# Kernel tuning notes

Measured on AMD Instinct MI355X. Metric: run time of the kernel, lower is better.

Reference implementation:

```python
import jax, jax.numpy as jnp
import numpy as np

HID, OUT = 128, 16
N_USER, N_MOVIE, N_DIR = 200000, 100000, 20000
ALPHA, NUM_LAYERS = 0.01, 2


def _seg_mean(h_src, src, dst, n_dst):
    # copy_u + mean reduce: mean of incoming messages per dst node (0 if no in-edges)
    msg = h_src[src]                                   # [E, H] gather
    s = jax.ops.segment_sum(msg, dst, num_segments=n_dst)
    deg = jax.ops.segment_sum(jnp.ones((dst.shape[0],), h_src.dtype), dst, num_segments=n_dst)
    return s / jnp.maximum(deg, 1.0)[:, None]


def setup_inputs() -> dict:
    key = jax.random.key(0)
    ks = jax.random.split(key, 16)
    inp = {
        'x_user': jax.random.normal(ks[0], (N_USER, 128), jnp.float32),
        'x_movie': jax.random.normal(ks[1], (N_MOVIE, 128), jnp.float32),
        'x_director': jax.random.normal(ks[2], (N_DIR, 128), jnp.float32),
        'rates_src': jax.random.randint(ks[3], (600000,), 0, N_USER, jnp.int32),
        'rates_dst': jax.random.randint(ks[4], (600000,), 0, N_MOVIE, jnp.int32),
        'rby_src': jax.random.randint(ks[5], (600000,), 0, N_MOVIE, jnp.int32),
        'rby_dst': jax.random.randint(ks[6], (600000,), 0, N_USER, jnp.int32),
        'dir_src': jax.random.randint(ks[7], (100000,), 0, N_DIR, jnp.int32),
        'dir_dst': jax.random.randint(ks[8], (100000,), 0, N_MOVIE, jnp.int32),
        'dby_src': jax.random.randint(ks[9], (100000,), 0, N_MOVIE, jnp.int32),
        'dby_dst': jax.random.randint(ks[10], (100000,), 0, N_DIR, jnp.int32),
    }
    sc = 1.0 / np.sqrt(128.0)
    inp['W_user'] = jax.random.normal(ks[11], (HID, 128), jnp.float32) * sc
    inp['b_user'] = jnp.zeros((HID,), jnp.float32)
    inp['W_movie'] = jax.random.normal(ks[12], (HID, 128), jnp.float32) * sc
    inp['b_movie'] = jnp.zeros((HID,), jnp.float32)
    inp['W_director'] = jax.random.normal(ks[13], (HID, 128), jnp.float32) * sc
    inp['b_director'] = jnp.zeros((HID,), jnp.float32)
    inp['W_out'] = jax.random.normal(ks[14], (OUT, HID), jnp.float32) * (1.0 / np.sqrt(HID))
    inp['b_out'] = jnp.zeros((OUT,), jnp.float32)
    return inp


def reference(x_user, x_movie, x_director,
              W_user, b_user, W_movie, b_movie, W_director, b_director,
              W_out, b_out,
              rates_src, rates_dst, rby_src, rby_dst,
              dir_src, dir_dst, dby_src, dby_dst):
    # per-ntype input Linear + ReLU (num_lins = 1)
    h_u = jax.nn.relu(x_user @ W_user.T + b_user)
    h_m = jax.nn.relu(x_movie @ W_movie.T + b_movie)
    h_d = jax.nn.relu(x_director @ W_director.T + b_director)
    for _ in range(NUM_LAYERS):
        # per-etype segment-mean; cross_reducer='mean' over etypes targeting each ntype
        agg_m = 0.5 * (_seg_mean(h_u, rates_src, rates_dst, N_MOVIE)
                       + _seg_mean(h_d, dir_src, dir_dst, N_MOVIE))
        agg_u = _seg_mean(h_m, rby_src, rby_dst, N_USER)
        agg_d = _seg_mean(h_m, dby_src, dby_dst, N_DIR)
        h_u = ALPHA * h_u + agg_u
        h_m = ALPHA * h_m + agg_m
        h_d = ALPHA * h_d + agg_d
    return h_m @ W_out.T + b_out  # target ntype 'movie' logits [N_MOVIE, OUT]
```

## Files before the change

### kernel.cpp

```cpp
#include <hip/hip_runtime.h>

#define ALPHA 0.01f
#define BIN_SHIFT 10
#define SBIN 1024

typedef __attribute__((ext_vector_type(8))) short short8v;
typedef __attribute__((ext_vector_type(4))) float float4v;

__device__ __forceinline__ void bsplit(float x, unsigned short& hi, unsigned short& lo) {
  unsigned u = __float_as_uint(x);
  hi = (unsigned short)(u >> 16);
  float r = x - __uint_as_float(u & 0xFFFF0000u);
  lo = (unsigned short)(__float_as_uint(r) >> 16);
}

__device__ __forceinline__ void frag_from8(const float* v, short8v& hi, short8v& lo) {
#pragma unroll
  for (int e = 0; e < 8; ++e) {
    unsigned short h, l;
    bsplit(v[e], h, l);
    hi[e] = (short)h;
    lo[e] = (short)l;
  }
}

__global__ __launch_bounds__(256, 2) void fused_mfma3_kernel(
    const float* __restrict__ Xu, const float* __restrict__ Xm, const float* __restrict__ Xd,
    const float* __restrict__ Wu, const float* __restrict__ Wm, const float* __restrict__ Wd,
    const float* __restrict__ Bu, const float* __restrict__ Bm, const float* __restrict__ Bd,
    const float* __restrict__ Wo,
    float* __restrict__ Gu, float* __restrict__ Gm, float* __restrict__ Gd,
    int NU, int NM, int ND, int bu, int bm)
{
  __shared__ char smem[65536 + 10368] __attribute__((aligned(16)));
  unsigned short* Whi = (unsigned short*)smem;
  unsigned short* Wlo = (unsigned short*)(smem + 32768);
  unsigned short* WoHi = (unsigned short*)(smem + 65536);
  unsigned short* WoLo = (unsigned short*)(smem + 65536 + 4096);

  const float *X, *W, *B;
  float* G;
  int N, bid, nbk;
  if ((int)blockIdx.x < bu)            { X = Xu; W = Wu; B = Bu; G = Gu; N = NU; bid = blockIdx.x;            nbk = bu; }
  else if ((int)blockIdx.x < bu + bm)  { X = Xm; W = Wm; B = Bm; G = Gm; N = NM; bid = blockIdx.x - bu;       nbk = bm; }
  else                                 { X = Xd; W = Wd; B = Bd; G = Gd; N = ND; bid = blockIdx.x - bu - bm;  nbk = gridDim.x - bu - bm; }

  const int t = threadIdx.x;
  const int wave = t >> 6;
  const int lane = t & 63;
  const int s = lane & 15;
  const int q = lane >> 4;
  float* hbuf = (float*)(smem + 65536 + wave * 2176);

#pragma unroll
  for (int i = 0; i < 32; ++i) {
    int p = i * 256 + t;
    int row = p >> 6, c2 = p & 63;
    float w0 = W[row * 128 + c2 * 2];
    float w1 = W[row * 128 + c2 * 2 + 1];
    unsigned short h0, l0, h1, l1;
    bsplit(w0, h0, l0); bsplit(w1, h1, l1);
    int u32idx = row * 64 + ((((c2 * 4) ^ ((row & 7) << 4))) >> 2);
    ((unsigned*)Whi)[u32idx] = (unsigned)h0 | ((unsigned)h1 << 16);
    ((unsigned*)Wlo)[u32idx] = (unsigned)l0 | ((unsigned)l1 << 16);
  }
#pragma unroll
  for (int i = 0; i < 4; ++i) {
    int p = i * 256 + t;
    int row = p >> 6, c2 = p & 63;
    float w0 = Wo[row * 128 + c2 * 2];
    float w1 = Wo[row * 128 + c2 * 2 + 1];
    unsigned short h0, l0, h1, l1;
    bsplit(w0, h0, l0); bsplit(w1, h1, l1);
    int u32idx = row * 64 + ((((c2 * 4) ^ ((row & 7) << 4))) >> 2);
    ((unsigned*)WoHi)[u32idx] = (unsigned)h0 | ((unsigned)h1 << 16);
    ((unsigned*)WoLo)[u32idx] = (unsigned)l0 | ((unsigned)l1 << 16);
  }
  __syncthreads();

  short8v woh[4], wol[4];
  const int woswz = (s & 7) << 4;
#pragma unroll
  for (int ks = 0; ks < 4; ++ks) {
    int off = s * 256 + ((ks * 64 + q * 16) ^ woswz);
    woh[ks] = *(const short8v*)((char*)WoHi + off);
    wol[ks] = *(const short8v*)((char*)WoLo + off);
  }
  float bv[8];
#pragma unroll
  for (int nt = 0; nt < 8; ++nt) bv[nt] = B[nt * 16 + s];
  __syncthreads();

  const int nchunks = (N + 127) >> 7;
  const int bswz = (s & 7) << 4;

  for (int chunk = bid; chunk < nchunks; chunk += nbk) {
    const int rowbase = chunk * 128 + wave * 32;

    short8v ahi[2][4], alo[2][4];
#pragma unroll
    for (int mt = 0; mt < 2; ++mt) {
      int row = rowbase + mt * 16 + s;
      int crow = row < N ? row : (N - 1);
      const float* xr = X + (size_t)crow * 128;
#pragma unroll
      for (int ks = 0; ks < 4; ++ks) {
        float4 f0 = *(const float4*)(xr + ks * 32 + q * 8);
        float4 f1 = *(const float4*)(xr + ks * 32 + q * 8 + 4);
        float v[8] = {f0.x, f0.y, f0.z, f0.w, f1.x, f1.y, f1.z, f1.w};
        frag_from8(v, ahi[mt][ks], alo[mt][ks]);
      }
    }

    float4v acc[2][8];
#pragma unroll
    for (int mt = 0; mt < 2; ++mt)
#pragma unroll
      for (int nt = 0; nt < 8; ++nt) acc[mt][nt] = (float4v){0.f, 0.f, 0.f, 0.f};

#pragma unroll
    for (int ks = 0; ks < 4; ++ks) {
      short8v bh[8];
#pragma unroll
      for (int nt = 0; nt < 8; ++nt) {
        int c = nt * 16 + s;
        int off = c * 256 + ((ks * 64 + q * 16) ^ bswz);
        bh[nt] = *(const short8v*)((char*)Whi + off);
      }
#pragma unroll
      for (int nt = 0; nt < 8; ++nt) {
#pragma unroll
        for (int mt = 0; mt < 2; ++mt) {
          acc[mt][nt] = __builtin_amdgcn_mfma_f32_16x16x32_bf16(ahi[mt][ks], bh[nt], acc[mt][nt], 0, 0, 0);
          acc[mt][nt] = __builtin_amdgcn_mfma_f32_16x16x32_bf16(alo[mt][ks], bh[nt], acc[mt][nt], 0, 0, 0);
        }
      }
#pragma unroll
      for (int nt = 0; nt < 8; ++nt) {
        int c = nt * 16 + s;
        int off = c * 256 + ((ks * 64 + q * 16) ^ bswz);
        short8v bl = *(const short8v*)((char*)Wlo + off);
#pragma unroll
        for (int mt = 0; mt < 2; ++mt)
          acc[mt][nt] = __builtin_amdgcn_mfma_f32_16x16x32_bf16(ahi[mt][ks], bl, acc[mt][nt], 0, 0, 0);
      }
    }

#pragma unroll
    for (int mt = 0; mt < 2; ++mt) {
      float4v gacc = (float4v){0.f, 0.f, 0.f, 0.f};
#pragma unroll
      for (int ks = 0; ks < 4; ++ks) {
#pragma unroll
        for (int j = 0; j < 2; ++j) {
          int nt = 2 * ks + j;
          int cl = j * 16 + s;
#pragma unroll
          for (int e = 0; e < 4; ++e)
            hbuf[cl * 17 + q * 4 + e] = fmaxf(acc[mt][nt][e] + bv[nt], 0.f);
        }
        float hv[8];
#pragma unroll
        for (int e = 0; e < 8; ++e) hv[e] = hbuf[(q * 8 + e) * 17 + s];
        short8v hh, hl;
        frag_from8(hv, hh, hl);
        gacc = __builtin_amdgcn_mfma_f32_16x16x32_bf16(hh, woh[ks], gacc, 0, 0, 0);
        gacc = __builtin_amdgcn_mfma_f32_16x16x32_bf16(hl, woh[ks], gacc, 0, 0, 0);
        gacc = __builtin_amdgcn_mfma_f32_16x16x32_bf16(hh, wol[ks], gacc, 0, 0, 0);
      }
      int grow = rowbase + mt * 16 + 4 * q;
#pragma unroll
      for (int e = 0; e < 4; ++e)
        if (grow + e < N) G[(size_t)(grow + e) * 16 + s] = gacc[e];
    }
  }
}

__device__ __forceinline__ void edge_decode(
    int i, const int* ys, const int* yd, int Erby,
    const int* bs, const int* bd, int Edby,
    const int* rs, const int* rd, int Er,
    const int* ds, const int* dd,
    int NU, int& src, int& bucket, int& bin)
{
  if (i < Erby)            { src = ys[i]; bucket = yd[i];                 bin = bucket >> BIN_SHIFT; }
  else if (i < Erby + Edby){ int j = i - Erby; src = bs[j]; bucket = NU + bd[j]; bin = bucket >> BIN_SHIFT; }
  else if (i < Erby + Edby + Er) { int j = i - Erby - Edby; src = rs[j]; bucket = 2 * rd[j]; bin = 256 + (bucket >> BIN_SHIFT); }
  else                     { int j = i - Erby - Edby - Er; src = ds[j]; bucket = 2 * dd[j] + 1; bin = 256 + (bucket >> BIN_SHIFT); }
}

__global__ __launch_bounds__(256) void hist2_kernel(
    const int* __restrict__ ys, const int* __restrict__ yd, int Erby,
    const int* __restrict__ bs, const int* __restrict__ bd, int Edby,
    const int* __restrict__ rs, const int* __restrict__ rd, int Er,
    const int* __restrict__ ds, const int* __restrict__ dd, int Edir,
    int NU, int* __restrict__ binHist)
{
  __shared__ int h[512];
  h[threadIdx.x] = 0; h[threadIdx.x + 256] = 0;
  __syncthreads();
  const int E = Erby + Edby + Er + Edir;
  for (int i = blockIdx.x * 256 + threadIdx.x; i < E; i += gridDim.x * 256) {
    int src, bucket, bin;
    edge_decode(i, ys, yd, Erby, bs, bd, Edby, rs, rd, Er, ds, dd, NU, src, bucket, bin);
    atomicAdd(&h[bin], 1);
  }
  __syncthreads();
  int v0 = h[threadIdx.x], v1 = h[threadIdx.x + 256];
  if (v0) atomicAdd(&binHist[threadIdx.x], v0);
  if (v1) atomicAdd(&binHist[threadIdx.x + 256], v1);
}

__global__ __launch_bounds__(256) void scan2s_kernel(
    const int* __restrict__ binHist, int* __restrict__ binStartA,
    int* __restrict__ binStartB, int* __restrict__ cursor)
{
  __shared__ int tmp[256];
  const int t = threadIdx.x;
#pragma unroll
  for (int stage = 0; stage < 2; ++stage) {
    int v = binHist[stage * 256 + t];
    tmp[t] = v;
    __syncthreads();
    for (int d = 1; d < 256; d <<= 1) {
      int add = (t >= d) ? tmp[t - d] : 0;
      __syncthreads();
      tmp[t] += add;
      __syncthreads();
    }
    int excl = tmp[t] - v;
    int* bs = stage ? binStartB : binStartA;
    bs[t] = excl;
    cursor[stage * 256 + t] = excl;
    if (t == 255) bs[256] = tmp[255];
    __syncthreads();
  }
}

__global__ __launch_bounds__(256) void fill2_kernel(
    const int* __restrict__ ys, const int* __restrict__ yd, int Erby,
    const int* __restrict__ bs, const int* __restrict__ bd, int Edby,
    const int* __restrict__ rs, const int* __restrict__ rd, int Er,
    const int* __restrict__ ds, const int* __restrict__ dd, int Edir,
    int NU, int* __restrict__ cursor,
    unsigned* __restrict__ binnedA, unsigned* __restrict__ binnedB)
{
  __shared__ int h[512];
  __shared__ int base[512];
  const int E = Erby + Edby + Er + Edir;
  const int c0 = blockIdx.x * 4096;
  const int c1 = (c0 + 4096 < E) ? c0 + 4096 : E;
  h[threadIdx.x] = 0; h[threadIdx.x + 256] = 0;
  __syncthreads();
  for (int i = c0 + threadIdx.x; i < c1; i += 256) {
    int src, bucket, bin;
    edge_decode(i, ys, yd, Erby, bs, bd, Edby, rs, rd, Er, ds, dd, NU, src, bucket, bin);
    atomicAdd(&h[bin], 1);
  }
  __syncthreads();
#pragma unroll
  for (int k = threadIdx.x; k < 512; k += 256) {
    int c = h[k];
    base[k] = c ? atomicAdd(&cursor[k], c) : 0;
    h[k] = 0;
  }
  __syncthreads();
  for (int i = c0 + threadIdx.x; i < c1; i += 256) {
    int src, bucket, bin;
    edge_decode(i, ys, yd, Erby, bs, bd, Edby, rs, rd, Er, ds, dd, NU, src, bucket, bin);
    int r = atomicAdd(&h[bin], 1);
    unsigned code = ((unsigned)src << BIN_SHIFT) | (unsigned)(bucket & (SBIN - 1));
    if (bin < 256) binnedA[base[bin] + r] = code;
    else           binnedB[base[bin] + r] = code;
  }
}

__global__ __launch_bounds__(256) void scatter2_kernel(
    const unsigned* __restrict__ binnedA, const int* __restrict__ binStartA, int nbinsA, int HA,
    const unsigned* __restrict__ binnedB, const int* __restrict__ binStartB, int HB,
    int* __restrict__ bOffsA, int* __restrict__ bCntA,
    int* __restrict__ bOffsB, int* __restrict__ bCntB,
    int* __restrict__ ssrcA, int* __restrict__ ssrcB)
{
  __shared__ int cnt[SBIN];
  __shared__ int pref[SBIN];
  __shared__ int wsum[256];
  const int t = threadIdx.x;
  const unsigned* binned; const int* binStart;
  int* bOffs; int* bCnt; int* ssrc;
  int b, nbuckets;
  if ((int)blockIdx.x < nbinsA) {
    b = blockIdx.x; binned = binnedA; binStart = binStartA;
    bOffs = bOffsA; bCnt = bCntA; ssrc = ssrcA; nbuckets = HA;
  } else {
    b = blockIdx.x - nbinsA; binned = binnedB; binStart = binStartB;
    bOffs = bOffsB; bCnt = bCntB; ssrc = ssrcB; nbuckets = HB;
  }
  const int s0 = binStart[b], s1 = binStart[b + 1];
#pragma unroll
  for (int k = t; k < SBIN; k += 256) cnt[k] = 0;
  __syncthreads();
  for (int i = s0 + t; i < s1; i += 256)
    atomicAdd(&cnt[binned[i] & (SBIN - 1)], 1);
  __syncthreads();
  int c0 = cnt[4 * t], c1 = cnt[4 * t + 1], c2 = cnt[4 * t + 2], c3 = cnt[4 * t + 3];
  int s = c0 + c1 + c2 + c3;
  wsum[t] = s;
  __syncthreads();
  for (int d = 1; d < 256; d <<= 1) {
    int add = (t >= d) ? wsum[t - d] : 0;
    __syncthreads();
    wsum[t] += add;
    __syncthreads();
  }
  int base = wsum[t] - s;
  pref[4 * t]     = base;
  pref[4 * t + 1] = base + c0;
  pref[4 * t + 2] = base + c0 + c1;
  pref[4 * t + 3] = base + c0 + c1 + c2;
  __syncthreads();
  const int gb = b << BIN_SHIFT;
#pragma unroll
  for (int k = t; k < SBIN; k += 256) {
    int bucket = gb + k;
    if (bucket < nbuckets) { bOffs[bucket] = s0 + pref[k]; bCnt[bucket] = cnt[k]; }
  }
  __syncthreads();
#pragma unroll
  for (int k = t; k < SBIN; k += 256) cnt[k] = pref[k];
  __syncthreads();
  for (int i = s0 + t; i < s1; i += 256) {
    unsigned code = binned[i];
    int local = code & (SBIN - 1);
    int r = atomicAdd(&cnt[local], 1);
    ssrc[s0 + r] = (int)(code >> BIN_SHIFT);
  }
}

__global__ __launch_bounds__(256) void gather_pay2_kernel(
    const float* __restrict__ g_m, const float* __restrict__ g_u,
    const float* __restrict__ g_d,
    const int* __restrict__ bOffsA, const int* __restrict__ bCntA,
    const int* __restrict__ ssrcA,
    float* __restrict__ pay_u, float* __restrict__ pay_d, int NU, int ND)
{
  int tid = blockIdx.x * 256 + threadIdx.x;
  int node = tid >> 4, o = tid & 15;
  if (node >= NU + ND) return;
  int start = bOffsA[node], cnt = bCntA[node];
  float sum = 0.f;
  for (int j = 0; j < cnt; ++j) {
    int s = ssrcA[start + j];
    sum += g_m[(size_t)s * 16 + o];
  }
  float mean = 0.5f * sum / fmaxf((float)cnt, 1.f);
  if (node < NU)
    pay_u[(size_t)node * 16 + o] = ALPHA * g_u[(size_t)node * 16 + o] + mean;
  else {
    int nn = node - NU;
    pay_d[(size_t)nn * 16 + o] = ALPHA * g_d[(size_t)nn * 16 + o] + mean;
  }
}

__global__ __launch_bounds__(256) void final_kernel(
    const float* __restrict__ gm, const float* __restrict__ pay_u,
    const float* __restrict__ pay_d,
    const int* __restrict__ bOffs, const int* __restrict__ bCnt,
    const int* __restrict__ ssrc,
    const float* __restrict__ bo, float* __restrict__ out, int NM)
{
  int tid = blockIdx.x * 256 + threadIdx.x;
  int m = tid >> 4, o = tid & 15;
  if (m >= NM) return;
  int s0 = bOffs[2 * m], c0 = bCnt[2 * m];
  float sr = 0.f;
  for (int j = 0; j < c0; ++j) sr += pay_u[(size_t)ssrc[s0 + j] * 16 + o];
  int s1 = bOffs[2 * m + 1], c1 = bCnt[2 * m + 1];
  float sd = 0.f;
  for (int j = 0; j < c1; ++j) sd += pay_d[(size_t)ssrc[s1 + j] * 16 + o];
  out[(size_t)m * 16 + o] = bo[o] + ALPHA * ALPHA * gm[(size_t)m * 16 + o]
                          + sr / fmaxf((float)c0, 1.f) + sd / fmaxf((float)c1, 1.f);
}

extern "C" void kernel_launch(void* const* d_in, const int* in_sizes, int n_in,
                              void* d_out, int out_size, void* d_ws, size_t ws_size,
                              hipStream_t stream)
{
  const float* x_user  = (const float*)d_in[0];
  const float* x_movie = (const float*)d_in[1];
  const float* x_dir   = (const float*)d_in[2];
  const int* rates_src = (const int*)d_in[3];
  const int* rates_dst = (const int*)d_in[4];
  const int* rby_src   = (const int*)d_in[5];
  const int* rby_dst   = (const int*)d_in[6];
  const int* dir_src   = (const int*)d_in[7];
  const int* dir_dst   = (const int*)d_in[8];
  const int* dby_src   = (const int*)d_in[9];
  const int* dby_dst   = (const int*)d_in[10];
  const float* W_user  = (const float*)d_in[11];
  const float* b_user  = (const float*)d_in[12];
  const float* W_movie = (const float*)d_in[13];
  const float* b_movie = (const float*)d_in[14];
  const float* W_dir   = (const float*)d_in[15];
  const float* b_dir   = (const float*)d_in[16];
  const float* W_out   = (const float*)d_in[17];
  const float* b_out   = (const float*)d_in[18];

  const int NU = in_sizes[0] / 128, NM = in_sizes[1] / 128, ND = in_sizes[2] / 128;
  const int Er = in_sizes[3], Erby = in_sizes[5], Edir = in_sizes[7], Edby = in_sizes[9];

  const int EA = Erby + Edby;
  const int EB = Er + Edir;
  const int E  = EA + EB;
  const int HA = NU + ND;
  const int HB = 2 * NM;
  const int nbinsA = (HA + SBIN - 1) >> BIN_SHIFT;
  const int nbinsB = (HB + SBIN - 1) >> BIN_SHIFT;

  char* w = (char*)d_ws;
  size_t off = 0;
  auto take = [&](size_t bytes) { char* p = w + off; off += (bytes + 255) & ~(size_t)255; return p; };
  float* g_u   = (float*)take((size_t)NU * 16 * 4);
  float* g_m   = (float*)take((size_t)NM * 16 * 4);
  float* g_d   = (float*)take((size_t)ND * 16 * 4);
  float* pay_u = (float*)take((size_t)NU * 16 * 4);
  float* pay_d = (float*)take((size_t)ND * 16 * 4);
  int* binHist    = (int*)take(512 * 4);
  int* binStartA  = (int*)take(257 * 4);
  int* binStartB  = (int*)take(257 * 4);
  int* cursor     = (int*)take(512 * 4);
  int* bOffsA     = (int*)take((size_t)HA * 4);
  int* bCntA      = (int*)take((size_t)HA * 4);
  int* bOffsB     = (int*)take((size_t)HB * 4);
  int* bCntB      = (int*)take((size_t)HB * 4);
  unsigned* binnedA = (unsigned*)take((size_t)EA * 4);
  unsigned* binnedB = (unsigned*)take((size_t)EB * 4);
  int* ssrcA      = (int*)take((size_t)EA * 4);
  int* ssrcB      = (int*)take((size_t)EB * 4);
  if (off > ws_size) return;

  hipMemsetAsync(binHist, 0, 512 * 4, stream);

  hist2_kernel<<<512, 256, 0, stream>>>(
      rby_src, rby_dst, Erby, dby_src, dby_dst, Edby,
      rates_src, rates_dst, Er, dir_src, dir_dst, Edir, NU, binHist);

  scan2s_kernel<<<1, 256, 0, stream>>>(binHist, binStartA, binStartB, cursor);

  fill2_kernel<<<(E + 4095) / 4096, 256, 0, stream>>>(
      rby_src, rby_dst, Erby, dby_src, dby_dst, Edby,
      rates_src, rates_dst, Er, dir_src, dir_dst, Edir, NU,
      cursor, binnedA, binnedB);

  scatter2_kernel<<<nbinsA + nbinsB, 256, 0, stream>>>(
      binnedA, binStartA, nbinsA, HA, binnedB, binStartB, HB,
      bOffsA, bCntA, bOffsB, bCntB, ssrcA, ssrcB);

  {
    long long cu = (NU + 127) >> 7, cm = (NM + 127) >> 7, cd = (ND + 127) >> 7;
    long long ct = cu + cm + cd;
    int bu = (int)((512 * cu + ct / 2) / ct);
    int bm = (int)((512 * cm + ct / 2) / ct);
    if (bu < 1) bu = 1;
    if (bm < 1) bm = 1;
    if (bu + bm > 510) { bu = 510 * bu / (bu + bm); bm = 510 - bu; }
    fused_mfma3_kernel<<<512, 256, 0, stream>>>(
        x_user, x_movie, x_dir, W_user, W_movie, W_dir,
        b_user, b_movie, b_dir, W_out, g_u, g_m, g_d,
        NU, NM, ND, bu, bm);
  }

  gather_pay2_kernel<<<((NU + ND) * 16 + 255) / 256, 256, 0, stream>>>(
      g_m, g_u, g_d, bOffsA, bCntA, ssrcA, pay_u, pay_d, NU, ND);

  final_kernel<<<(NM * 16 + 255) / 256, 256, 0, stream>>>(
      g_m, pay_u, pay_d, bOffsB, bCntB, ssrcB, b_out, (float*)d_out, NM);
}
```

Measured before the change: 176.0 us.

## Co-schedule MFMA projection blocks with fill and scatter CSR-build kernels

Splits the fused per-ntype projection GEMM into a device body and launches it inside the fill and scatter kernels as extra blocks. Movie projections run alongside the fill pass and user/director projections alongside the scatter pass, so the compute-bound GEMM overlaps the memory/atomic-bound graph preprocessing and two launches go away. It also prefetches the next chunk's X rows into registers (software pipelining) and changes the hbuf padding stride from 17 to 19. The cost is higher register pressure and a larger shared-memory footprint for the fill and scatter blocks, which may reduce their occupancy.

New measurement: 316.2 us. 79.6% more time.

```diff
diff --git a/kernel.cpp b/kernel.cpp
--- a/kernel.cpp
+++ b/kernel.cpp
@@ -6,6 +6,8 @@
 
 typedef __attribute__((ext_vector_type(8))) short short8v;
 typedef __attribute__((ext_vector_type(4))) float float4v;
+
+#define SMEM_BYTES 75264
 
 __device__ __forceinline__ void bsplit(float x, unsigned short& hi, unsigned short& lo) {
   unsigned u = __float_as_uint(x);
@@ -24,33 +26,21 @@
   }
 }
 
-__global__ __launch_bounds__(256, 2) void fused_mfma3_kernel(
-    const float* __restrict__ Xu, const float* __restrict__ Xm, const float* __restrict__ Xd,
-    const float* __restrict__ Wu, const float* __restrict__ Wm, const float* __restrict__ Wd,
-    const float* __restrict__ Bu, const float* __restrict__ Bm, const float* __restrict__ Bd,
-    const float* __restrict__ Wo,
-    float* __restrict__ Gu, float* __restrict__ Gm, float* __restrict__ Gd,
-    int NU, int NM, int ND, int bu, int bm)
-{
-  __shared__ char smem[65536 + 10368] __attribute__((aligned(16)));
+__device__ void mfma_body(const float* __restrict__ X, const float* __restrict__ W,
+                          const float* __restrict__ B, const float* __restrict__ Wo,
+                          float* __restrict__ G, int N, int bid, int nbk, char* smem)
+{
   unsigned short* Whi = (unsigned short*)smem;
   unsigned short* Wlo = (unsigned short*)(smem + 32768);
   unsigned short* WoHi = (unsigned short*)(smem + 65536);
   unsigned short* WoLo = (unsigned short*)(smem + 65536 + 4096);
-
-  const float *X, *W, *B;
-  float* G;
-  int N, bid, nbk;
-  if ((int)blockIdx.x < bu)            { X = Xu; W = Wu; B = Bu; G = Gu; N = NU; bid = blockIdx.x;            nbk = bu; }
-  else if ((int)blockIdx.x < bu + bm)  { X = Xm; W = Wm; B = Bm; G = Gm; N = NM; bid = blockIdx.x - bu;       nbk = bm; }
-  else                                 { X = Xd; W = Wd; B = Bd; G = Gd; N = ND; bid = blockIdx.x - bu - bm;  nbk = gridDim.x - bu - bm; }
 
   const int t = threadIdx.x;
   const int wave = t >> 6;
   const int lane = t & 63;
   const int s = lane & 15;
   const int q = lane >> 4;
-  float* hbuf = (float*)(smem + 65536 + wave * 2176);
+  float* hbuf = (float*)(smem + 65536 + wave * 2432);
 
 #pragma unroll
   for (int i = 0; i < 32; ++i) {
@@ -94,10 +84,9 @@
   const int nchunks = (N + 127) >> 7;
   const int bswz = (s & 7) << 4;
 
-  for (int chunk = bid; chunk < nchunks; chunk += nbk) {
+  float4 xraw[16];
+  auto load_x = [&](int chunk) {
     const int rowbase = chunk * 128 + wave * 32;
-
-    short8v ahi[2][4], alo[2][4];
 #pragma unroll
     for (int mt = 0; mt < 2; ++mt) {
       int row = rowbase + mt * 16 + s;
@@ -105,12 +94,26 @@
       const float* xr = X + (size_t)crow * 128;
 #pragma unroll
       for (int ks = 0; ks < 4; ++ks) {
-        float4 f0 = *(const float4*)(xr + ks * 32 + q * 8);
-        float4 f1 = *(const float4*)(xr + ks * 32 + q * 8 + 4);
+        xraw[mt * 8 + ks * 2]     = *(const float4*)(xr + ks * 32 + q * 8);
+        xraw[mt * 8 + ks * 2 + 1] = *(const float4*)(xr + ks * 32 + q * 8 + 4);
+      }
+    }
+  };
+
+  if (bid < nchunks) load_x(bid);
+
+  for (int chunk = bid; chunk < nchunks; chunk += nbk) {
+    short8v ahi[2][4], alo[2][4];
+#pragma unroll
+    for (int mt = 0; mt < 2; ++mt)
+#pragma unroll
+      for (int ks = 0; ks < 4; ++ks) {
+        float4 f0 = xraw[mt * 8 + ks * 2], f1 = xraw[mt * 8 + ks * 2 + 1];
         float v[8] = {f0.x, f0.y, f0.z, f0.w, f1.x, f1.y, f1.z, f1.w};
         frag_from8(v, ahi[mt][ks], alo[mt][ks]);
       }
-    }
+    int nxt = chunk + nbk;
+    if (nxt < nchunks) load_x(nxt);
 
     float4v acc[2][8];
 #pragma unroll
@@ -146,6 +149,7 @@
       }
     }
 
+    const int rowbase = chunk * 128 + wave * 32;
 #pragma unroll
     for (int mt = 0; mt < 2; ++mt) {
       float4v gacc = (float4v){0.f, 0.f, 0.f, 0.f};
@@ -157,11 +161,11 @@
           int cl = j * 16 + s;
 #pragma unroll
           for (int e = 0; e < 4; ++e)
-            hbuf[cl * 17 + q * 4 + e] = fmaxf(acc[mt][nt][e] + bv[nt], 0.f);
+            hbuf[cl * 19 + q * 4 + e] = fmaxf(acc[mt][nt][e] + bv[nt], 0.f);
         }
         float hv[8];
 #pragma unroll
-        for (int e = 0; e < 8; ++e) hv[e] = hbuf[(q * 8 + e) * 17 + s];
+        for (int e = 0; e < 8; ++e) hv[e] = hbuf[(q * 8 + e) * 19 + s];
         short8v hh, hl;
         frag_from8(hv, hh, hl);
         gacc = __builtin_amdgcn_mfma_f32_16x16x32_bf16(hh, woh[ks], gacc, 0, 0, 0);
@@ -237,18 +241,19 @@
   }
 }
 
-__global__ __launch_bounds__(256) void fill2_kernel(
+__device__ void fill_body(
     const int* __restrict__ ys, const int* __restrict__ yd, int Erby,
     const int* __restrict__ bs, const int* __restrict__ bd, int Edby,
     const int* __restrict__ rs, const int* __restrict__ rd, int Er,
     const int* __restrict__ ds, const int* __restrict__ dd, int Edir,
     int NU, int* __restrict__ cursor,
-    unsigned* __restrict__ binnedA, unsigned* __restrict__ binnedB)
-{
-  __shared__ int h[512];
-  __shared__ int base[512];
+    unsigned* __restrict__ binnedA, unsigned* __restrict__ binnedB,
+    int bid, char* smem)
+{
+  int* h    = (int*)smem;
+  int* base = (int*)(smem + 2048);
   const int E = Erby + Edby + Er + Edir;
-  const int c0 = blockIdx.x * 4096;
+  const int c0 = bid * 4096;
   const int c1 = (c0 + 4096 < E) ? c0 + 4096 : E;
   h[threadIdx.x] = 0; h[threadIdx.x + 256] = 0;
   __syncthreads();
@@ -275,25 +280,25 @@
   }
 }
 
-__global__ __launch_bounds__(256) void scatter2_kernel(
+__device__ void scatter_body(
     const unsigned* __restrict__ binnedA, const int* __restrict__ binStartA, int nbinsA, int HA,
     const unsigned* __restrict__ binnedB, const int* __restrict__ binStartB, int HB,
     int* __restrict__ bOffsA, int* __restrict__ bCntA,
     int* __restrict__ bOffsB, int* __restrict__ bCntB,
-    int* __restrict__ ssrcA, int* __restrict__ ssrcB)
-{
-  __shared__ int cnt[SBIN];
-  __shared__ int pref[SBIN];
-  __shared__ int wsum[256];
+    int* __restrict__ ssrcA, int* __restrict__ ssrcB, int bidx, char* smem)
+{
+  int* cnt  = (int*)smem;
+  int* pref = (int*)(smem + 4096);
+  int* wsum = (int*)(smem + 8192);
   const int t = threadIdx.x;
   const unsigned* binned; const int* binStart;
   int* bOffs; int* bCnt; int* ssrc;
   int b, nbuckets;
-  if ((int)blockIdx.x < nbinsA) {
-    b = blockIdx.x; binned = binnedA; binStart = binStartA;
+  if (bidx < nbinsA) {
+    b = bidx; binned = binnedA; binStart = binStartA;
     bOffs = bOffsA; bCnt = bCntA; ssrc = ssrcA; nbuckets = HA;
   } else {
-    b = blockIdx.x - nbinsA; binned = binnedB; binStart = binStartB;
+    b = bidx - nbinsA; binned = binnedB; binStart = binStartB;
     bOffs = bOffsB; bCnt = bCntB; ssrc = ssrcB; nbuckets = HB;
   }
   const int s0 = binStart[b], s1 = binStart[b + 1];
@@ -334,6 +339,48 @@
     int local = code & (SBIN - 1);
     int r = atomicAdd(&cnt[local], 1);
     ssrc[s0 + r] = (int)(code >> BIN_SHIFT);
+  }
+}
+
+__global__ __launch_bounds__(256, 2) void fill_mfmaM_kernel(
+    const int* __restrict__ ys, const int* __restrict__ yd, int Erby,
+    const int* __restrict__ bs, const int* __restrict__ bd, int Edby,
+    const int* __restrict__ rs, const int* __restrict__ rd, int Er,
+    const int* __restrict__ ds, const int* __restrict__ dd, int Edir,
+    int NU, int* __restrict__ cursor,
+    unsigned* __restrict__ binnedA, unsigned* __restrict__ binnedB, int nf,
+    const float* __restrict__ Xm, const float* __restrict__ Wm,
+    const float* __restrict__ Bm, const float* __restrict__ Wo,
+    float* __restrict__ Gm, int NM)
+{
+  __shared__ char smem[SMEM_BYTES] __attribute__((aligned(16)));
+  if ((int)blockIdx.x < nf)
+    fill_body(ys, yd, Erby, bs, bd, Edby, rs, rd, Er, ds, dd, Edir, NU,
+              cursor, binnedA, binnedB, blockIdx.x, smem);
+  else
+    mfma_body(Xm, Wm, Bm, Wo, Gm, NM, blockIdx.x - nf, gridDim.x - nf, smem);
+}
+
+__global__ __launch_bounds__(256, 2) void scatter_mfmaUD_kernel(
+    const unsigned* __restrict__ binnedA, const int* __restrict__ binStartA, int nbinsA, int HA,
+    const unsigned* __restrict__ binnedB, const int* __restrict__ binStartB, int HB,
+    int* __restrict__ bOffsA, int* __restrict__ bCntA,
+    int* __restrict__ bOffsB, int* __restrict__ bCntB,
+    int* __restrict__ ssrcA, int* __restrict__ ssrcB, int nsc, int bu,
+    const float* __restrict__ Xu, const float* __restrict__ Wu, const float* __restrict__ Bu,
+    const float* __restrict__ Xd, const float* __restrict__ Wd, const float* __restrict__ Bd,
+    const float* __restrict__ Wo, float* __restrict__ Gu, float* __restrict__ Gd,
+    int NU, int ND)
+{
+  __shared__ char smem[SMEM_BYTES] __attribute__((aligned(16)));
+  if ((int)blockIdx.x < nsc)
+    scatter_body(binnedA, binStartA, nbinsA, HA, binnedB, binStartB, HB,
+                 bOffsA, bCntA, bOffsB, bCntB, ssrcA, ssrcB, blockIdx.x, smem);
+  else {
+    int b = blockIdx.x - nsc;
+    int nmf = gridDim.x - nsc;
+    if (b < bu) mfma_body(Xu, Wu, Bu, Wo, Gu, NU, b, bu, smem);
+    else        mfma_body(Xd, Wd, Bd, Wo, Gd, ND, b - bu, nmf - bu, smem);
   }
 }
 
@@ -447,27 +494,25 @@
 
   scan2s_kernel<<<1, 256, 0, stream>>>(binHist, binStartA, binStartB, cursor);
 
-  fill2_kernel<<<(E + 4095) / 4096, 256, 0, stream>>>(
+  const int nf = (E + 4095) / 4096;
+  fill_mfmaM_kernel<<<nf + 256, 256, 0, stream>>>(
       rby_src, rby_dst, Erby, dby_src, dby_dst, Edby,
       rates_src, rates_dst, Er, dir_src, dir_dst, Edir, NU,
-      cursor, binnedA, binnedB);
-
-  scatter2_kernel<<<nbinsA + nbinsB, 256, 0, stream>>>(
-      binnedA, binStartA, nbinsA, HA, binnedB, binStartB, HB,
-      bOffsA, bCntA, bOffsB, bCntB, ssrcA, ssrcB);
+      cursor, binnedA, binnedB, nf,
+      x_movie, W_movie, b_movie, W_out, g_m, NM);
 
   {
-    long long cu = (NU + 127) >> 7, cm = (NM + 127) >> 7, cd = (ND + 127) >> 7;
-    long long ct = cu + cm + cd;
-    int bu = (int)((512 * cu + ct / 2) / ct);
-    int bm = (int)((512 * cm + ct / 2) / ct);
+    const int nsc = nbinsA + nbinsB;
+    const int NMF = 384;
+    long long cu = (NU + 127) >> 7, cd = (ND + 127) >> 7;
+    int bu = (int)(((long long)NMF * cu + (cu + cd) / 2) / (cu + cd));
     if (bu < 1) bu = 1;
-    if (bm < 1) bm = 1;
-    if (bu + bm > 510) { bu = 510 * bu / (bu + bm); bm = 510 - bu; }
-    fused_mfma3_kernel<<<512, 256, 0, stream>>>(
-        x_user, x_movie, x_dir, W_user, W_movie, W_dir,
-        b_user, b_movie, b_dir, W_out, g_u, g_m, g_d,
-        NU, NM, ND, bu, bm);
+    if (bu > NMF - 1) bu = NMF - 1;
+    scatter_mfmaUD_kernel<<<nsc + NMF, 256, 0, stream>>>(
+        binnedA, binStartA, nbinsA, HA, binnedB, binStartB, HB,
+        bOffsA, bCntA, bOffsB, bCntB, ssrcA, ssrcB, nsc, bu,
+        x_user, W_user, b_user, x_dir, W_dir, b_dir, W_out,
+        g_u, g_d, NU, ND);
   }
 
   gather_pay2_kernel<<<((NU + ND) * 16 + 255) / 256, 256, 0, stream>>>(
```

## Replace histogram/scan binning with fixed-capacity bins and fuse gather into scatter

Applied to the files above, without the earlier changes.

Drops the histogram and scan kernels by giving each coarse bin a fixed-capacity window of CAPB slots, with the per-bin cursor counting edges directly from zero. It also folds the user/director payload gather into the per-bin scatter kernel, so the A-side offset and count arrays no longer need to be written. This removes two launches and one global pass over the edges. In exchange the A-side gather runs with far fewer threads, one block per bin walking 1024 buckets, and any bin holding more than CAPB edges silently loses edges.

Measured after the change: 370.0 us. 110% more time.

```diff
diff --git a/kernel.cpp b/kernel.cpp
--- a/kernel.cpp
+++ b/kernel.cpp
@@ -3,6 +3,7 @@
 #define ALPHA 0.01f
 #define BIN_SHIFT 10
 #define SBIN 1024
+#define CAPB 8192
 
 typedef __attribute__((ext_vector_type(8))) short short8v;
 typedef __attribute__((ext_vector_type(4))) float float4v;
@@ -189,54 +190,6 @@
   else                     { int j = i - Erby - Edby - Er; src = ds[j]; bucket = 2 * dd[j] + 1; bin = 256 + (bucket >> BIN_SHIFT); }
 }
 
-__global__ __launch_bounds__(256) void hist2_kernel(
-    const int* __restrict__ ys, const int* __restrict__ yd, int Erby,
-    const int* __restrict__ bs, const int* __restrict__ bd, int Edby,
-    const int* __restrict__ rs, const int* __restrict__ rd, int Er,
-    const int* __restrict__ ds, const int* __restrict__ dd, int Edir,
-    int NU, int* __restrict__ binHist)
-{
-  __shared__ int h[512];
-  h[threadIdx.x] = 0; h[threadIdx.x + 256] = 0;
-  __syncthreads();
-  const int E = Erby + Edby + Er + Edir;
-  for (int i = blockIdx.x * 256 + threadIdx.x; i < E; i += gridDim.x * 256) {
-    int src, bucket, bin;
-    edge_decode(i, ys, yd, Erby, bs, bd, Edby, rs, rd, Er, ds, dd, NU, src, bucket, bin);
-    atomicAdd(&h[bin], 1);
-  }
-  __syncthreads();
-  int v0 = h[threadIdx.x], v1 = h[threadIdx.x + 256];
-  if (v0) atomicAdd(&binHist[threadIdx.x], v0);
-  if (v1) atomicAdd(&binHist[threadIdx.x + 256], v1);
-}
-
-__global__ __launch_bounds__(256) void scan2s_kernel(
-    const int* __restrict__ binHist, int* __restrict__ binStartA,
-    int* __restrict__ binStartB, int* __restrict__ cursor)
-{
-  __shared__ int tmp[256];
-  const int t = threadIdx.x;
-#pragma unroll
-  for (int stage = 0; stage < 2; ++stage) {
-    int v = binHist[stage * 256 + t];
-    tmp[t] = v;
-    __syncthreads();
-    for (int d = 1; d < 256; d <<= 1) {
-      int add = (t >= d) ? tmp[t - d] : 0;
-      __syncthreads();
-      tmp[t] += add;
-      __syncthreads();
-    }
-    int excl = tmp[t] - v;
-    int* bs = stage ? binStartB : binStartA;
-    bs[t] = excl;
-    cursor[stage * 256 + t] = excl;
-    if (t == 255) bs[256] = tmp[255];
-    __syncthreads();
-  }
-}
-
 __global__ __launch_bounds__(256) void fill2_kernel(
     const int* __restrict__ ys, const int* __restrict__ yd, int Erby,
     const int* __restrict__ bs, const int* __restrict__ bd, int Edby,
@@ -269,39 +222,41 @@
     int src, bucket, bin;
     edge_decode(i, ys, yd, Erby, bs, bd, Edby, rs, rd, Er, ds, dd, NU, src, bucket, bin);
     int r = atomicAdd(&h[bin], 1);
-    unsigned code = ((unsigned)src << BIN_SHIFT) | (unsigned)(bucket & (SBIN - 1));
-    if (bin < 256) binnedA[base[bin] + r] = code;
-    else           binnedB[base[bin] + r] = code;
-  }
-}
-
-__global__ __launch_bounds__(256) void scatter2_kernel(
-    const unsigned* __restrict__ binnedA, const int* __restrict__ binStartA, int nbinsA, int HA,
-    const unsigned* __restrict__ binnedB, const int* __restrict__ binStartB, int HB,
-    int* __restrict__ bOffsA, int* __restrict__ bCntA,
+    int pos = base[bin] + r;
+    if (pos < CAPB) {
+      unsigned code = ((unsigned)src << BIN_SHIFT) | (unsigned)(bucket & (SBIN - 1));
+      if (bin < 256) binnedA[(size_t)bin * CAPB + pos] = code;
+      else           binnedB[(size_t)(bin - 256) * CAPB + pos] = code;
+    }
+  }
+}
+
+__global__ __launch_bounds__(256) void scatter_pay_kernel(
+    const unsigned* __restrict__ binnedA, const unsigned* __restrict__ binnedB,
+    const int* __restrict__ cursor, int nbinsA, int HA, int HB,
     int* __restrict__ bOffsB, int* __restrict__ bCntB,
-    int* __restrict__ ssrcA, int* __restrict__ ssrcB)
+    int* __restrict__ ssrcA, int* __restrict__ ssrcB,
+    const float* __restrict__ g_m, const float* __restrict__ g_u,
+    const float* __restrict__ g_d,
+    float* __restrict__ pay_u, float* __restrict__ pay_d, int NU, int ND)
 {
   __shared__ int cnt[SBIN];
   __shared__ int pref[SBIN];
   __shared__ int wsum[256];
   const int t = threadIdx.x;
-  const unsigned* binned; const int* binStart;
-  int* bOffs; int* bCnt; int* ssrc;
-  int b, nbuckets;
-  if ((int)blockIdx.x < nbinsA) {
-    b = blockIdx.x; binned = binnedA; binStart = binStartA;
-    bOffs = bOffsA; bCnt = bCntA; ssrc = ssrcA; nbuckets = HA;
-  } else {
-    b = blockIdx.x - nbinsA; binned = binnedB; binStart = binStartB;
-    bOffs = bOffsB; bCnt = bCntB; ssrc = ssrcB; nbuckets = HB;
-  }
-  const int s0 = binStart[b], s1 = binStart[b + 1];
+  const bool isA = (int)blockIdx.x < nbinsA;
+  const int b = isA ? (int)blockIdx.x : (int)blockIdx.x - nbinsA;
+  const unsigned* win = (isA ? binnedA : binnedB) + (size_t)b * CAPB;
+  int* ssrc = isA ? ssrcA : ssrcB;
+  const size_t wbase = (size_t)b * CAPB;
+  int n = cursor[isA ? b : 256 + b];
+  if (n > CAPB) n = CAPB;
+
 #pragma unroll
   for (int k = t; k < SBIN; k += 256) cnt[k] = 0;
   __syncthreads();
-  for (int i = s0 + t; i < s1; i += 256)
-    atomicAdd(&cnt[binned[i] & (SBIN - 1)], 1);
+  for (int i = t; i < n; i += 256)
+    atomicAdd(&cnt[win[i] & (SBIN - 1)], 1);
   __syncthreads();
   int c0 = cnt[4 * t], c1 = cnt[4 * t + 1], c2 = cnt[4 * t + 2], c3 = cnt[4 * t + 3];
   int s = c0 + c1 + c2 + c3;
@@ -320,45 +275,43 @@
   pref[4 * t + 3] = base + c0 + c1 + c2;
   __syncthreads();
   const int gb = b << BIN_SHIFT;
-#pragma unroll
-  for (int k = t; k < SBIN; k += 256) {
-    int bucket = gb + k;
-    if (bucket < nbuckets) { bOffs[bucket] = s0 + pref[k]; bCnt[bucket] = cnt[k]; }
+  if (!isA) {
+#pragma unroll
+    for (int k = t; k < SBIN; k += 256) {
+      int bucket = gb + k;
+      if (bucket < HB) { bOffsB[bucket] = (int)(wbase + pref[k]); bCntB[bucket] = cnt[k]; }
+    }
   }
   __syncthreads();
 #pragma unroll
   for (int k = t; k < SBIN; k += 256) cnt[k] = pref[k];
   __syncthreads();
-  for (int i = s0 + t; i < s1; i += 256) {
-    unsigned code = binned[i];
+  for (int i = t; i < n; i += 256) {
+    unsigned code = win[i];
     int local = code & (SBIN - 1);
     int r = atomicAdd(&cnt[local], 1);
-    ssrc[s0 + r] = (int)(code >> BIN_SHIFT);
-  }
-}
-
-__global__ __launch_bounds__(256) void gather_pay2_kernel(
-    const float* __restrict__ g_m, const float* __restrict__ g_u,
-    const float* __restrict__ g_d,
-    const int* __restrict__ bOffsA, const int* __restrict__ bCntA,
-    const int* __restrict__ ssrcA,
-    float* __restrict__ pay_u, float* __restrict__ pay_d, int NU, int ND)
-{
-  int tid = blockIdx.x * 256 + threadIdx.x;
-  int node = tid >> 4, o = tid & 15;
-  if (node >= NU + ND) return;
-  int start = bOffsA[node], cnt = bCntA[node];
-  float sum = 0.f;
-  for (int j = 0; j < cnt; ++j) {
-    int s = ssrcA[start + j];
-    sum += g_m[(size_t)s * 16 + o];
-  }
-  float mean = 0.5f * sum / fmaxf((float)cnt, 1.f);
-  if (node < NU)
-    pay_u[(size_t)node * 16 + o] = ALPHA * g_u[(size_t)node * 16 + o] + mean;
-  else {
-    int nn = node - NU;
-    pay_d[(size_t)nn * 16 + o] = ALPHA * g_d[(size_t)nn * 16 + o] + mean;
+    ssrc[wbase + r] = (int)(code >> BIN_SHIFT);
+  }
+
+  if (isA) {
+    __syncthreads();
+    const int o = t & 15, g = t >> 4;
+    for (int k = g; k < SBIN; k += 16) {
+      int bucket = gb + k;
+      if (bucket >= HA) break;
+      int ck = cnt[k] - pref[k];
+      size_t start = wbase + pref[k];
+      float sum = 0.f;
+      for (int j = 0; j < ck; ++j) {
+        int src = ssrcA[start + j];
+        sum += g_m[(size_t)src * 16 + o];
+      }
+      float mean = 0.5f * sum / fmaxf((float)ck, 1.f);
+      if (bucket < NU)
+        pay_u[(size_t)bucket * 16 + o] = ALPHA * g_u[(size_t)bucket * 16 + o] + mean;
+      else
+        pay_d[(size_t)(bucket - NU) * 16 + o] = ALPHA * g_d[(size_t)(bucket - NU) * 16 + o] + mean;
+    }
   }
 }
 
@@ -409,9 +362,7 @@
   const int NU = in_sizes[0] / 128, NM = in_sizes[1] / 128, ND = in_sizes[2] / 128;
   const int Er = in_sizes[3], Erby = in_sizes[5], Edir = in_sizes[7], Edby = in_sizes[9];
 
-  const int EA = Erby + Edby;
-  const int EB = Er + Edir;
-  const int E  = EA + EB;
+  const int E  = Er + Edir + Erby + Edby;
   const int HA = NU + ND;
   const int HB = 2 * NM;
   const int nbinsA = (HA + SBIN - 1) >> BIN_SHIFT;
@@ -425,36 +376,21 @@
   float* g_d   = (float*)take((size_t)ND * 16 * 4);
   float* pay_u = (float*)take((size_t)NU * 16 * 4);
   float* pay_d = (float*)take((size_t)ND * 16 * 4);
-  int* binHist    = (int*)take(512 * 4);
-  int* binStartA  = (int*)take(257 * 4);
-  int* binStartB  = (int*)take(257 * 4);
   int* cursor     = (int*)take(512 * 4);
-  int* bOffsA     = (int*)take((size_t)HA * 4);
-  int* bCntA      = (int*)take((size_t)HA * 4);
   int* bOffsB     = (int*)take((size_t)HB * 4);
   int* bCntB      = (int*)take((size_t)HB * 4);
-  unsigned* binnedA = (unsigned*)take((size_t)EA * 4);
-  unsigned* binnedB = (unsigned*)take((size_t)EB * 4);
-  int* ssrcA      = (int*)take((size_t)EA * 4);
-  int* ssrcB      = (int*)take((size_t)EB * 4);
+  unsigned* binnedA = (unsigned*)take((size_t)nbinsA * CAPB * 4);
+  unsigned* binnedB = (unsigned*)take((size_t)nbinsB * CAPB * 4);
+  int* ssrcA      = (int*)take((size_t)nbinsA * CAPB * 4);
+  int* ssrcB      = (int*)take((size_t)nbinsB * CAPB * 4);
   if (off > ws_size) return;
 
-  hipMemsetAsync(binHist, 0, 512 * 4, stream);
-
-  hist2_kernel<<<512, 256, 0, stream>>>(
-      rby_src, rby_dst, Erby, dby_src, dby_dst, Edby,
-      rates_src, rates_dst, Er, dir_src, dir_dst, Edir, NU, binHist);
-
-  scan2s_kernel<<<1, 256, 0, stream>>>(binHist, binStartA, binStartB, cursor);
+  hipMemsetAsync(cursor, 0, 512 * 4, stream);
 
   fill2_kernel<<<(E + 4095) / 4096, 256, 0, stream>>>(
       rby_src, rby_dst, Erby, dby_src, dby_dst, Edby,
       rates_src, rates_dst, Er, dir_src, dir_dst, Edir, NU,
       cursor, binnedA, binnedB);
-
-  scatter2_kernel<<<nbinsA + nbinsB, 256, 0, stream>>>(
-      binnedA, binStartA, nbinsA, HA, binnedB, binStartB, HB,
-      bOffsA, bCntA, bOffsB, bCntB, ssrcA, ssrcB);
 
   {
     long long cu = (NU + 127) >> 7, cm = (NM + 127) >> 7, cd = (ND + 127) >> 7;
@@ -470,8 +406,10 @@
         NU, NM, ND, bu, bm);
   }
 
-  gather_pay2_kernel<<<((NU + ND) * 16 + 255) / 256, 256, 0, stream>>>(
-      g_m, g_u, g_d, bOffsA, bCntA, ssrcA, pay_u, pay_d, NU, ND);
+  scatter_pay_kernel<<<nbinsA + nbinsB, 256, 0, stream>>>(
+      binnedA, binnedB, cursor, nbinsA, HA, HB,
+      bOffsB, bCntB, ssrcA, ssrcB,
+      g_m, g_u, g_d, pay_u, pay_d, NU, ND);
 
   final_kernel<<<(NM * 16 + 255) / 256, 256, 0, stream>>>(
       g_m, pay_u, pay_d, bOffsB, bCntB, ssrcB, b_out, (float*)d_out, NM);
```
